# Performance work log

Hardware: AMD Instinct MI355X
Metric: run time of the kernel (lower is better)

The kernel has to match this reference:

```python
import jax, jax.numpy as jnp
import numpy as np

N_NODES = 9
NEG_SLOPE = 0.2
# static edge list from the module (src, dst) pairs, PyG convention row0=src, row1=dst
_E = np.array([[0,1],[1,0],[0,3],[3,0],[0,5],[5,0],[0,7],[7,0],
               [1,2],[2,1],[3,4],[4,3],[5,6],[6,5],[7,8],[8,7]], dtype=np.int32).T
# GATv2Conv default add_self_loops=True
SRC = jnp.asarray(np.concatenate([_E[0], np.arange(N_NODES, dtype=np.int32)]))
DST = jnp.asarray(np.concatenate([_E[1], np.arange(N_NODES, dtype=np.int32)]))


def setup_inputs() -> dict:
    key = jax.random.key(0)
    k1, k2, k3, k4 = jax.random.split(key, 4)
    B, C_IN, C_OUT = 16384, 256, 256
    scale = 1.0 / np.sqrt(C_IN)
    return {
        "x": jax.random.normal(k1, (B, N_NODES, C_IN), jnp.float32),
        "W_l": jax.random.normal(k2, (C_IN, C_OUT), jnp.float32) * scale,
        "W_r": jax.random.normal(k3, (C_IN, C_OUT), jnp.float32) * scale,
        "att": jax.random.normal(k4, (C_OUT,), jnp.float32) * scale,
        "bias": jnp.zeros((C_OUT,), jnp.float32),
    }


def reference(x, W_l, W_r, att, bias):
    # x: [B, N, C_in] batch of identical small graphs
    xl = jnp.einsum("bnc,cd->bnd", x, W_l)  # source-side projection
    xr = jnp.einsum("bnc,cd->bnd", x, W_r)  # target-side projection
    # per-edge GATv2 score: a^T LeakyReLU(x_l[src] + x_r[dst])
    e = jax.nn.leaky_relu(xl[:, SRC] + xr[:, DST], NEG_SLOPE)  # [B, E, C_out]
    score = jnp.einsum("bed,d->be", e, att)                    # [B, E]
    # softmax over incoming edges of each destination node (segment softmax)
    sT = score.T                                               # [E, B]
    m = jax.ops.segment_max(sT, DST, num_segments=N_NODES)     # [N, B]
    ex = jnp.exp(sT - m[DST])
    denom = jax.ops.segment_sum(ex, DST, num_segments=N_NODES)
    alpha = ex / denom[DST]                                    # [E, B]
    # scatter-aggregate messages alpha * x_l[src] into dst
    msg = xl[:, SRC] * alpha.T[..., None]                      # [B, E, C_out]
    out = jax.ops.segment_sum(msg.transpose(1, 0, 2), DST, num_segments=N_NODES)
    return out.transpose(1, 0, 2) + bias                       # [B, N, C_out]
```

## Files before the change

### kernel.cpp

```cpp
#include <hip/hip_runtime.h>
#include <hip/hip_bf16.h>

typedef __attribute__((ext_vector_type(8))) short short8;
typedef __attribute__((ext_vector_type(4))) float f32x4;
typedef __attribute__((ext_vector_type(2))) float f32x2;
typedef __attribute__((ext_vector_type(4))) unsigned short u16x4;

#define STAGE_BYTES (80 * 512)
#define ALPHA_OFF   (8 * 25 * 8 * 4)

__device__ __forceinline__ unsigned short f2bf(float f) {
    unsigned int u = __float_as_uint(f);
    unsigned int r = (u + 0x7fffu + ((u >> 16) & 1u)) >> 16;
    return (unsigned short)r;
}

constexpr int C_SRC[25] = {0,1,0,3,0,5,0,7,1,2,3,4,5,6,7,8, 0,1,2,3,4,5,6,7,8};
constexpr int C_DST[25] = {1,0,3,0,5,0,7,0,2,1,4,3,6,5,8,7, 0,1,2,3,4,5,6,7,8};
constexpr int C_NINC[9]  = {5,3,2,3,2,3,2,3,2};
constexpr int C_IOFF[9]  = {0,5,8,10,13,15,18,20,23};
constexpr int C_INCE[25] = {1,3,5,7,16, 0,9,17, 8,18, 2,11,19, 10,20, 4,13,21, 12,22, 6,15,23, 14,24};
constexpr int C_INCS[25] = {1,3,5,7,0,  0,2,1,  1,2,  0,4,3,  3,4,  0,6,5,  5,6,  0,8,7,  7,8};
__device__ const int D_NINC[9]  = {5,3,2,3,2,3,2,3,2};
__device__ const int D_IOFF[9]  = {0,5,8,10,13,15,18,20,23};
__device__ const int D_INCE[25] = {1,3,5,7,16, 0,9,17, 8,18, 2,11,19, 10,20, 4,13,21, 12,22, 6,15,23, 14,24};

__global__ void convert_w_kernel(const float* __restrict__ Wl,
                                 const float* __restrict__ Wr,
                                 unsigned short* __restrict__ WT) {
    int n = blockIdx.x;
    int k = threadIdx.x;
    float v = (n < 256) ? Wl[k * 256 + n] : Wr[k * 256 + (n - 256)];
    WT[n * 256 + k] = f2bf(v);
}

__global__ __launch_bounds__(512, 4) void gat_fused_kernel(
        const float* __restrict__ x,
        const unsigned short* __restrict__ WT,
        const float* __restrict__ att,
        const float* __restrict__ bias,
        float* __restrict__ out) {
    __shared__ __align__(16) char smem[STAGE_BYTES];
    float* partials = (float*)smem;
    float* alphas   = (float*)(smem + ALPHA_OFF);

    const int tid  = threadIdx.x;
    const int lane = tid & 63;
    const int w    = tid >> 6;
    const int gl   = lane >> 4;
    const int li   = lane & 15;
    const int blk  = blockIdx.x;

    const int c0 = 32 * w + li, c1 = c0 + 16;
    const float attc0 = att[c0], attc1 = att[c1];
    const float bc0   = bias[c0], bc1 = bias[c1];

    const float* xblk = x + (size_t)blk * 18432;
    {
        f32x4 xv[9];
        #pragma unroll
        for (int it = 0; it < 9; ++it)
            xv[it] = *(const f32x4*)(xblk + it * 2048 + tid * 4);
        #pragma unroll
        for (int it = 0; it < 9; ++it) {
            int f    = it * 2048 + tid * 4;
            int gr   = f >> 8;
            int c    = f & 255;
            int g    = gr / 9;
            int node = gr - g * 9;
            int key  = 2 * g + (node & 1);
            int srow = ((node >> 1) << 4) + key;
            u16x4 pk = { f2bf(xv[it][0]), f2bf(xv[it][1]), f2bf(xv[it][2]), f2bf(xv[it][3]) };
            *(u16x4*)(smem + srow * 512 + ((2 * c) ^ (key << 4))) = pk;
        }
    }
    __syncthreads();

    const unsigned short* WL = WT + (size_t)(c0 * 256 + gl * 8);
    const unsigned short* WR = WL + 256 * 256;
    const f32x4 ZERO = {0.f, 0.f, 0.f, 0.f};

    f32x4 aL[5][2], aR[5][2];

    #pragma unroll
    for (int m = 0; m < 5; ++m) { aL[m][0] = ZERO; aL[m][1] = ZERO; }
    #pragma unroll
    for (int kc = 0; kc < 8; ++kc) {
        short8 bl0 = *(const short8*)(WL + kc * 32);
        short8 bl1 = *(const short8*)(WL + 4096 + kc * 32);
        const int inner = ((kc * 64) + (gl * 16)) ^ (li << 4);
        #pragma unroll
        for (int m = 0; m < 5; ++m) {
            short8 a = *(const short8*)(smem + (m * 16 + li) * 512 + inner);
            aL[m][0] = __builtin_amdgcn_mfma_f32_16x16x32_bf16(a, bl0, aL[m][0], 0, 0, 0);
            aL[m][1] = __builtin_amdgcn_mfma_f32_16x16x32_bf16(a, bl1, aL[m][1], 0, 0, 0);
        }
    }
    #pragma unroll
    for (int m = 0; m < 5; ++m) { aR[m][0] = ZERO; aR[m][1] = ZERO; }
    #pragma unroll
    for (int kc = 0; kc < 8; ++kc) {
        short8 br0 = *(const short8*)(WR + kc * 32);
        short8 br1 = *(const short8*)(WR + 4096 + kc * 32);
        const int inner = ((kc * 64) + (gl * 16)) ^ (li << 4);
        #pragma unroll
        for (int m = 0; m < 5; ++m) {
            short8 a = *(const short8*)(smem + (m * 16 + li) * 512 + inner);
            aR[m][0] = __builtin_amdgcn_mfma_f32_16x16x32_bf16(a, br0, aR[m][0], 0, 0, 0);
            aR[m][1] = __builtin_amdgcn_mfma_f32_16x16x32_bf16(a, br1, aR[m][1], 0, 0, 0);
        }
    }
    __syncthreads();

    #pragma unroll
    for (int e = 0; e < 25; ++e) {
        const int s = C_SRC[e], d = C_DST[e];
        const int mL = s >> 1, pL = s & 1;
        const int mR = d >> 1, pR = d & 1;
        float p0 = 0.f, p1 = 0.f;
        #pragma unroll
        for (int nt = 0; nt < 2; ++nt) {
            const float ac = nt ? attc1 : attc0;
            float v0 = aL[mL][nt][pL]     + aR[mR][nt][pR];
            float v1 = aL[mL][nt][2 + pL] + aR[mR][nt][2 + pR];
            p0 += ac * fmaxf(v0, 0.2f * v0);
            p1 += ac * fmaxf(v1, 0.2f * v1);
        }
        #pragma unroll
        for (int m = 1; m < 16; m <<= 1) {
            p0 += __shfl_xor(p0, m);
            p1 += __shfl_xor(p1, m);
        }
        if (li == 0) {
            f32x2 pk = {p0, p1};
            *(f32x2*)(partials + (w * 25 + e) * 8 + 2 * gl) = pk;
        }
    }
    __syncthreads();

    if (tid < 72) {
        int n = tid >> 3, g = tid & 7;
        int off = D_IOFF[n], cnt = D_NINC[n];
        float mx = -1e30f;
        for (int i = 0; i < cnt; ++i) {
            int e = D_INCE[off + i];
            float s = 0.f;
            #pragma unroll
            for (int ww = 0; ww < 8; ++ww) s += partials[(ww * 25 + e) * 8 + g];
            alphas[e * 8 + g] = s;
            mx = fmaxf(mx, s);
        }
        float ssum = 0.f;
        for (int i = 0; i < cnt; ++i)
            ssum += __expf(alphas[D_INCE[off + i] * 8 + g] - mx);
        float inv = 1.f / ssum;
        for (int i = 0; i < cnt; ++i) {
            int e = D_INCE[off + i];
            alphas[e * 8 + g] = __expf(alphas[e * 8 + g] - mx) * inv;
        }
    }
    __syncthreads();

    #pragma unroll
    for (int n = 0; n < 9; ++n) {
        float o00 = bc0, o01 = bc1;
        float o10 = bc0, o11 = bc1;
        #pragma unroll
        for (int i = 0; i < C_NINC[n]; ++i) {
            const int e  = C_INCE[C_IOFF[n] + i];
            const int sn = C_INCS[C_IOFF[n] + i];
            const int ms = sn >> 1, ps = sn & 1;
            f32x2 al = *(const f32x2*)(alphas + e * 8 + 2 * gl);
            o00 += al[0] * aL[ms][0][ps];
            o01 += al[0] * aL[ms][1][ps];
            o10 += al[1] * aL[ms][0][2 + ps];
            o11 += al[1] * aL[ms][1][2 + ps];
        }
        size_t row0 = ((size_t)blk * 8 + 2 * gl) * 9 + n;
        out[row0 * 256 + c0] = o00;
        out[row0 * 256 + c1] = o01;
        out[(row0 + 9) * 256 + c0] = o10;
        out[(row0 + 9) * 256 + c1] = o11;
    }
}

extern "C" void kernel_launch(void* const* d_in, const int* in_sizes, int n_in,
                              void* d_out, int out_size, void* d_ws, size_t ws_size,
                              hipStream_t stream) {
    const float* x    = (const float*)d_in[0];
    const float* Wl   = (const float*)d_in[1];
    const float* Wr   = (const float*)d_in[2];
    const float* att  = (const float*)d_in[3];
    const float* bias = (const float*)d_in[4];
    float* out = (float*)d_out;
    unsigned short* WT = (unsigned short*)d_ws;

    convert_w_kernel<<<512, 256, 0, stream>>>(Wl, Wr, WT);
    gat_fused_kernel<<<2048, 512, 0, stream>>>(x, WT, att, bias, out);
}
```

Measured before the change: 151.6 us.

## Split right projection by column tile to cut registers; use DPP reductions

Computes the right-side projection one 16-column tile at a time and consumes each tile right away in an edge-score pass. This halves the live accumulators for the right projection, and the partial scores are now stored per wave and per tile in a separate LDS region, so the staged x tile no longer needs a barrier before it is overwritten. The 16-lane reductions switch from shuffles to DPP row operations. In exchange the LDS A-fragments are read again for the second right tile, the score pass runs twice, and LDS use grows a little.

Measured after the change: 148.7 us. Within noise of the previous version (-1.9%).

```diff
diff --git a/kernel.cpp b/kernel.cpp
--- a/kernel.cpp
+++ b/kernel.cpp
@@ -7,12 +7,27 @@
 typedef __attribute__((ext_vector_type(4))) unsigned short u16x4;
 
 #define STAGE_BYTES (80 * 512)
-#define ALPHA_OFF   (8 * 25 * 8 * 4)
+#define PART_OFF    STAGE_BYTES
+#define ALPHA_OFF   (PART_OFF + 16 * 25 * 8 * 4)
+#define LDS_BYTES   (ALPHA_OFF + 25 * 8 * 4)
 
 __device__ __forceinline__ unsigned short f2bf(float f) {
     unsigned int u = __float_as_uint(f);
     unsigned int r = (u + 0x7fffu + ((u >> 16) & 1u)) >> 16;
     return (unsigned short)r;
+}
+
+template<int CTRL>
+__device__ __forceinline__ float dpp_add(float v) {
+    int p = __builtin_amdgcn_update_dpp(0, __float_as_int(v), CTRL, 0xf, 0xf, true);
+    return v + __int_as_float(p);
+}
+__device__ __forceinline__ float sum16(float v) {
+    v = dpp_add<0xB1>(v);
+    v = dpp_add<0x4E>(v);
+    v = dpp_add<0x141>(v);
+    v = dpp_add<0x140>(v);
+    return v;
 }
 
 constexpr int C_SRC[25] = {0,1,0,3,0,5,0,7,1,2,3,4,5,6,7,8, 0,1,2,3,4,5,6,7,8};
@@ -25,6 +40,27 @@
 __device__ const int D_IOFF[9]  = {0,5,8,10,13,15,18,20,23};
 __device__ const int D_INCE[25] = {1,3,5,7,16, 0,9,17, 8,18, 2,11,19, 10,20, 4,13,21, 12,22, 6,15,23, 14,24};
 
+template<int NT>
+__device__ __forceinline__ void edge_scores(const f32x4 (&aL)[5][2], const f32x4 (&aRt)[5],
+                                            float ac, float* pbase, int li) {
+    #pragma unroll
+    for (int e = 0; e < 25; ++e) {
+        const int s = C_SRC[e], d = C_DST[e];
+        const int mL = s >> 1, pL = s & 1;
+        const int mR = d >> 1, pR = d & 1;
+        float v0 = aL[mL][NT][pL]     + aRt[mR][pR];
+        float v1 = aL[mL][NT][2 + pL] + aRt[mR][2 + pR];
+        float p0 = ac * fmaxf(v0, 0.2f * v0);
+        float p1 = ac * fmaxf(v1, 0.2f * v1);
+        p0 = sum16(p0);
+        p1 = sum16(p1);
+        if (li == 0) {
+            f32x2 pk = {p0, p1};
+            *(f32x2*)(pbase + e * 8) = pk;
+        }
+    }
+}
+
 __global__ void convert_w_kernel(const float* __restrict__ Wl,
                                  const float* __restrict__ Wr,
                                  unsigned short* __restrict__ WT) {
@@ -40,8 +76,8 @@
         const float* __restrict__ att,
         const float* __restrict__ bias,
         float* __restrict__ out) {
-    __shared__ __align__(16) char smem[STAGE_BYTES];
-    float* partials = (float*)smem;
+    __shared__ __align__(16) char smem[LDS_BYTES];
+    float* partials = (float*)(smem + PART_OFF);
     float* alphas   = (float*)(smem + ALPHA_OFF);
 
     const int tid  = threadIdx.x;
@@ -80,61 +116,46 @@
     const unsigned short* WR = WL + 256 * 256;
     const f32x4 ZERO = {0.f, 0.f, 0.f, 0.f};
 
-    f32x4 aL[5][2], aR[5][2];
-
+    f32x4 aL[5][2];
     #pragma unroll
     for (int m = 0; m < 5; ++m) { aL[m][0] = ZERO; aL[m][1] = ZERO; }
-    #pragma unroll
-    for (int kc = 0; kc < 8; ++kc) {
-        short8 bl0 = *(const short8*)(WL + kc * 32);
-        short8 bl1 = *(const short8*)(WL + 4096 + kc * 32);
-        const int inner = ((kc * 64) + (gl * 16)) ^ (li << 4);
-        #pragma unroll
-        for (int m = 0; m < 5; ++m) {
-            short8 a = *(const short8*)(smem + (m * 16 + li) * 512 + inner);
-            aL[m][0] = __builtin_amdgcn_mfma_f32_16x16x32_bf16(a, bl0, aL[m][0], 0, 0, 0);
-            aL[m][1] = __builtin_amdgcn_mfma_f32_16x16x32_bf16(a, bl1, aL[m][1], 0, 0, 0);
-        }
-    }
-    #pragma unroll
-    for (int m = 0; m < 5; ++m) { aR[m][0] = ZERO; aR[m][1] = ZERO; }
-    #pragma unroll
-    for (int kc = 0; kc < 8; ++kc) {
-        short8 br0 = *(const short8*)(WR + kc * 32);
-        short8 br1 = *(const short8*)(WR + 4096 + kc * 32);
-        const int inner = ((kc * 64) + (gl * 16)) ^ (li << 4);
-        #pragma unroll
-        for (int m = 0; m < 5; ++m) {
-            short8 a = *(const short8*)(smem + (m * 16 + li) * 512 + inner);
-            aR[m][0] = __builtin_amdgcn_mfma_f32_16x16x32_bf16(a, br0, aR[m][0], 0, 0, 0);
-            aR[m][1] = __builtin_amdgcn_mfma_f32_16x16x32_bf16(a, br1, aR[m][1], 0, 0, 0);
-        }
-    }
-    __syncthreads();
-
-    #pragma unroll
-    for (int e = 0; e < 25; ++e) {
-        const int s = C_SRC[e], d = C_DST[e];
-        const int mL = s >> 1, pL = s & 1;
-        const int mR = d >> 1, pR = d & 1;
-        float p0 = 0.f, p1 = 0.f;
-        #pragma unroll
-        for (int nt = 0; nt < 2; ++nt) {
-            const float ac = nt ? attc1 : attc0;
-            float v0 = aL[mL][nt][pL]     + aR[mR][nt][pR];
-            float v1 = aL[mL][nt][2 + pL] + aR[mR][nt][2 + pR];
-            p0 += ac * fmaxf(v0, 0.2f * v0);
-            p1 += ac * fmaxf(v1, 0.2f * v1);
-        }
-        #pragma unroll
-        for (int m = 1; m < 16; m <<= 1) {
-            p0 += __shfl_xor(p0, m);
-            p1 += __shfl_xor(p1, m);
-        }
-        if (li == 0) {
-            f32x2 pk = {p0, p1};
-            *(f32x2*)(partials + (w * 25 + e) * 8 + 2 * gl) = pk;
-        }
+
+    {
+        f32x4 aRt[5];
+        #pragma unroll
+        for (int m = 0; m < 5; ++m) aRt[m] = ZERO;
+        #pragma unroll
+        for (int kc = 0; kc < 8; ++kc) {
+            short8 bl0 = *(const short8*)(WL + kc * 32);
+            short8 bl1 = *(const short8*)(WL + 4096 + kc * 32);
+            short8 br0 = *(const short8*)(WR + kc * 32);
+            const int inner = ((kc * 64) + (gl * 16)) ^ (li << 4);
+            #pragma unroll
+            for (int m = 0; m < 5; ++m) {
+                short8 a = *(const short8*)(smem + (m * 16 + li) * 512 + inner);
+                aL[m][0] = __builtin_amdgcn_mfma_f32_16x16x32_bf16(a, bl0, aL[m][0], 0, 0, 0);
+                aL[m][1] = __builtin_amdgcn_mfma_f32_16x16x32_bf16(a, bl1, aL[m][1], 0, 0, 0);
+                aRt[m]   = __builtin_amdgcn_mfma_f32_16x16x32_bf16(a, br0, aRt[m],   0, 0, 0);
+            }
+        }
+        edge_scores<0>(aL, aRt, attc0, partials + (w * 2 + 0) * 200 + 2 * gl, li);
+    }
+
+    {
+        f32x4 aRt[5];
+        #pragma unroll
+        for (int m = 0; m < 5; ++m) aRt[m] = ZERO;
+        #pragma unroll
+        for (int kc = 0; kc < 8; ++kc) {
+            short8 br1 = *(const short8*)(WR + 4096 + kc * 32);
+            const int inner = ((kc * 64) + (gl * 16)) ^ (li << 4);
+            #pragma unroll
+            for (int m = 0; m < 5; ++m) {
+                short8 a = *(const short8*)(smem + (m * 16 + li) * 512 + inner);
+                aRt[m] = __builtin_amdgcn_mfma_f32_16x16x32_bf16(a, br1, aRt[m], 0, 0, 0);
+            }
+        }
+        edge_scores<1>(aL, aRt, attc1, partials + (w * 2 + 1) * 200 + 2 * gl, li);
     }
     __syncthreads();
 
@@ -146,7 +167,7 @@
             int e = D_INCE[off + i];
             float s = 0.f;
             #pragma unroll
-            for (int ww = 0; ww < 8; ++ww) s += partials[(ww * 25 + e) * 8 + g];
+            for (int ww = 0; ww < 16; ++ww) s += partials[ww * 200 + e * 8 + g];
             alphas[e * 8 + g] = s;
             mx = fmaxf(mx, s);
         }
```
